# Kernel tuning notes

Hardware: AMD Instinct MI355X
Metric: run time of the kernel (lower is better)

The kernel has to match this reference:

```python
import jax, jax.numpy as jnp
import numpy as np

B = 32768
NUM_DENSE = 13
PAD_DENSE = 16  # 13 padded up to multiple of 8
T = 26          # number of categorical tables
V = 100000      # cardinality per table
E = 128         # embedding_dim
BOTTOM_DIMS = [512, 256, 128]
TOP_DIMS = [1024, 1024, 512, 256, 1]
N_FEAT = T + 1  # 27 feature vectors entering interaction
PAIR = N_FEAT * (N_FEAT - 1) // 2  # 351
TOP_IN = PAIR + E   # 479
TOP_PAD = 480       # padded to multiple of 8


def _glorot(key, fan_in, fan_out):
    s = np.sqrt(2.0 / (fan_in + fan_out))
    return jax.random.normal(key, (fan_in, fan_out), jnp.float32) * s


def setup_inputs() -> dict:
    key = jax.random.key(0)
    ks = jax.random.split(key, 32)
    inp = {
        "numerical": jax.random.normal(ks[0], (B, NUM_DENSE), jnp.float32),
        "cat_features": jax.random.randint(ks[1], (B, T), 0, V, jnp.int32),
        "emb_tables": jax.random.normal(ks[2], (T, V, E), jnp.float32) * 0.01,
    }
    # bottom MLP: 16 -> 512 -> 256 -> 128 (all relu)
    d_in = PAD_DENSE
    for i, d in enumerate(BOTTOM_DIMS):
        inp[f"bw{i}"] = _glorot(ks[3 + 2 * i], d_in, d)
        inp[f"bb{i}"] = jax.random.normal(ks[4 + 2 * i], (d,), jnp.float32) * np.sqrt(1.0 / d)
        d_in = d
    # top MLP: 480 -> 1024 -> 1024 -> 512 -> 256 -> 1 (relu except last)
    d_in = TOP_PAD
    for i, d in enumerate(TOP_DIMS):
        inp[f"tw{i}"] = _glorot(ks[12 + 2 * i], d_in, d)
        inp[f"tb{i}"] = jax.random.normal(ks[13 + 2 * i], (d,), jnp.float32) * np.sqrt(1.0 / d)
        d_in = d
    return inp


def reference(numerical, cat_features, emb_tables,
              bw0, bb0, bw1, bb1, bw2, bb2,
              tw0, tb0, tw1, tb1, tw2, tb2, tw3, tb3, tw4, tb4):
    b = numerical.shape[0]
    # --- bottom MLP (dense features padded with zeros to 16) ---
    x = jnp.pad(numerical, ((0, 0), (0, PAD_DENSE - NUM_DENSE)))
    for w, bias in ((bw0, bb0), (bw1, bb1), (bw2, bb2)):
        x = jax.nn.relu(x @ w + bias)
    bottom_out = x  # [B, E]
    # --- multi-table embedding gather: emb_tables[t][cat[:, t]] ---
    emb_out = jax.vmap(lambda tab, idx: tab[idx], in_axes=(0, 1), out_axes=1)(
        emb_tables, cat_features)  # [B, T, E]
    # --- dot interaction ---
    feats = jnp.concatenate([bottom_out[:, None, :], emb_out], axis=1)  # [B, 27, E]
    Z = jnp.einsum('bnd,bmd->bnm', feats, feats)  # [B, 27, 27]
    iu, ju = jnp.triu_indices(N_FEAT, k=1)
    pair = Z[:, iu, ju]  # [B, 351]
    x = jnp.concatenate(
        [bottom_out, pair, jnp.zeros((b, TOP_PAD - TOP_IN), feats.dtype)], axis=1)  # [B, 480]
    # --- top MLP (relu except last layer) ---
    tops = ((tw0, tb0), (tw1, tb1), (tw2, tb2), (tw3, tb3), (tw4, tb4))
    for i, (w, bias) in enumerate(tops):
        x = x @ w + bias
        if i < len(tops) - 1:
            x = jax.nn.relu(x)
    return x  # [B, 1] logits
```

## Files before the change

kernel.cpp:

```cpp
#include <hip/hip_runtime.h>

typedef __bf16 bf16;
typedef __bf16 bf16x4 __attribute__((ext_vector_type(4)));
typedef __bf16 bf16x8 __attribute__((ext_vector_type(8)));
typedef float f32x4 __attribute__((ext_vector_type(4)));

#define B_SZ 32768
#define T_CAT 26
#define V_SZ 100000
#define E_SZ 128

__device__ __forceinline__ void gload_lds16(const void* g, void* l) {
    __builtin_amdgcn_global_load_lds(
        (const __attribute__((address_space(1))) void*)g,
        (__attribute__((address_space(3))) void*)l, 16, 0, 0);
}

struct CJob { const float* W; bf16* Wt; int K, N, Kp, blk0, tk; };
struct CJobs { CJob j[7]; };

__global__ __launch_bounds__(256) void convw_all(CJobs js) {
    __shared__ bf16 tile[64][66];
    const int b = blockIdx.x;
    int ji = 0;
#pragma unroll
    for (int k = 1; k < 7; ++k)
        if (b >= js.j[k].blk0) ji = k;
    const CJob J = js.j[ji];
    const int local = b - J.blk0;
    const int tn = local / J.tk;
    const int tkk = local - tn * J.tk;

    const int t = threadIdx.x;
    const int lx = t & 63;
    const int gy = t >> 6;

#pragma unroll
    for (int kk = 0; kk < 16; ++kk) {
        const int k = tkk * 64 + kk * 4 + gy;
        const int n = tn * 64 + lx;
        const float v = (k < J.K) ? J.W[(long)k * J.N + n] : 0.0f;
        tile[lx][kk * 4 + gy] = (bf16)v;
    }
    __syncthreads();
#pragma unroll
    for (int nn = 0; nn < 16; ++nn) {
        const int nloc = nn * 4 + gy;
        const int n = tn * 64 + nloc;
        const int k = tkk * 64 + lx;
        J.Wt[(long)n * J.Kp + k] = tile[nloc][lx];
    }
}

__global__ __launch_bounds__(256) void make_xpad(const float* __restrict__ num,
                                                 bf16* __restrict__ xp) {
    const int idx = blockIdx.x * 256 + threadIdx.x;
    const int b = idx >> 6, c = idx & 63;
    xp[idx] = (bf16)((c < 13) ? num[(long)b * 13 + c] : 0.0f);
}

template <int RELU>
__global__ __launch_bounds__(256) void gemm_bt(const bf16* __restrict__ A,
                                               const bf16* __restrict__ Bt,
                                               const float* __restrict__ bias,
                                               bf16* __restrict__ C,
                                               int M, int N, int K) {
    __shared__ __align__(16) bf16 As[128 * 64];
    __shared__ __align__(16) bf16 Bs[128 * 64];
    const int t = threadIdx.x;
    const int lane = t & 63;
    const int w = t >> 6;
    const int wm = w >> 1, wn = w & 1;
    const long row0 = (long)blockIdx.y * 128;
    const long col0 = (long)blockIdx.x * 128;

    const int srow = t >> 3;
    const int scol = (t & 7) * 8;
    const bf16* Ag = A + (row0 + srow) * (long)K + scol;
    const bf16* Bg = Bt + (col0 + srow) * (long)K + scol;
    bf16* AsB = &As[w * 512];
    bf16* BsB = &Bs[w * 512];

    f32x4 acc[4][4] = {};

    for (int k0 = 0; k0 < K; k0 += 64) {
#pragma unroll
        for (int q = 0; q < 4; ++q) {
            gload_lds16(Ag + (long)q * 32 * K + k0, AsB + q * 2048);
            gload_lds16(Bg + (long)q * 32 * K + k0, BsB + q * 2048);
        }
        __syncthreads();
#pragma unroll
        for (int s = 0; s < 2; ++s) {
            bf16x8 af[4], bv[4];
#pragma unroll
            for (int i = 0; i < 4; ++i)
                af[i] = *(const bf16x8*)&As[(wm * 64 + i * 16 + (lane & 15)) * 64 +
                                            s * 32 + (lane >> 4) * 8];
#pragma unroll
            for (int j = 0; j < 4; ++j)
                bv[j] = *(const bf16x8*)&Bs[(wn * 64 + j * 16 + (lane & 15)) * 64 +
                                            s * 32 + (lane >> 4) * 8];
#pragma unroll
            for (int i = 0; i < 4; ++i)
#pragma unroll
                for (int j = 0; j < 4; ++j)
                    acc[i][j] = __builtin_amdgcn_mfma_f32_16x16x32_bf16(
                        af[i], bv[j], acc[i][j], 0, 0, 0);
        }
        __syncthreads();
    }

    const int r4 = (lane >> 4) * 4;
    const int cn = lane & 15;
#pragma unroll
    for (int j = 0; j < 4; ++j) {
        const long col = col0 + wn * 64 + j * 16 + cn;
        const float bj = bias[col];
#pragma unroll
        for (int i = 0; i < 4; ++i) {
#pragma unroll
            for (int r = 0; r < 4; ++r) {
                const long row = row0 + wm * 64 + i * 16 + r4 + r;
                float v = acc[i][j][r] + bj;
                if (RELU) v = v > 0.0f ? v : 0.0f;
                C[row * (long)N + col] = (bf16)v;
            }
        }
    }
}

template <int RELU>
__global__ __launch_bounds__(512, 2) void gemm256(const bf16* __restrict__ A,
                                                  const bf16* __restrict__ Bt,
                                                  const float* __restrict__ bias,
                                                  bf16* __restrict__ C,
                                                  int M, int N, int K, int nbx) {
    __shared__ __align__(16) bf16 lds[4 * 2 * 8192];
    const int t = threadIdx.x;
    const int lane = t & 63;
    const int w = t >> 6;
    const int wm = w >> 2, wn = w & 3;

    const int nwg = gridDim.x;
    const int qch = nwg >> 3;
    const int swz = ((int)blockIdx.x & 7) * qch + ((int)blockIdx.x >> 3);
    const int bx = swz % nbx, by = swz / nbx;
    const long row0 = (long)by * 256;
    const long col0 = (long)bx * 256;

    const int NT = K >> 5;

    const int lr = lane >> 2;
    const int dslot = lane & 3;
    const int lrow0 = (w * 2 + 0) * 16 + lr;
    const int lrow1 = (w * 2 + 1) * 16 + lr;
    const int sl0 = dslot ^ ((lrow0 >> 1) & 3);
    const int sl1 = dslot ^ ((lrow1 >> 1) & 3);
    const bf16* Ag0 = A + (row0 + lrow0) * (long)K + sl0 * 8;
    const bf16* Ag1 = A + (row0 + lrow1) * (long)K + sl1 * 8;
    const bf16* Bg0 = Bt + (col0 + lrow0) * (long)K + sl0 * 8;
    const bf16* Bg1 = Bt + (col0 + lrow1) * (long)K + sl1 * 8;
    const int ldsRow0 = (w * 2 + 0) * 512;
    const int ldsRow1 = (w * 2 + 1) * 512;

#define STAGE_A(buf, kt)                                                   \
    do {                                                                   \
        const int _k0 = (kt) << 5;                                         \
        gload_lds16(Ag0 + _k0, &lds[((buf) * 2 + 0) * 8192 + ldsRow0]);    \
        gload_lds16(Ag1 + _k0, &lds[((buf) * 2 + 0) * 8192 + ldsRow1]);    \
    } while (0)
#define STAGE_B(buf, kt)                                                   \
    do {                                                                   \
        const int _k0 = (kt) << 5;                                         \
        gload_lds16(Bg0 + _k0, &lds[((buf) * 2 + 1) * 8192 + ldsRow0]);    \
        gload_lds16(Bg1 + _k0, &lds[((buf) * 2 + 1) * 8192 + ldsRow1]);    \
    } while (0)

    const int cm = lane & 15;
    const int kc = lane >> 4;
    int aoff[8], boff[4];
#pragma unroll
    for (int i = 0; i < 8; ++i) {
        const int r = wm * 128 + i * 16 + cm;
        aoff[i] = r * 32 + (kc ^ ((r >> 1) & 3)) * 8;
    }
#pragma unroll
    for (int j = 0; j < 4; ++j) {
        const int n = wn * 64 + j * 16 + cm;
        boff[j] = n * 32 + (kc ^ ((n >> 1) & 3)) * 8;
    }

    f32x4 acc[8][4] = {};

    STAGE_A(0, 0); STAGE_B(0, 0);
    STAGE_A(1, 1); STAGE_B(1, 1);
    STAGE_A(2, 2); STAGE_B(2, 2);

    for (int tt = 0; tt < NT; ++tt) {
        const int rem = NT - 1 - tt;
        const int sb = (tt + 3) & 3;
        const int sk = tt + 3;

        if (rem >= 2)      asm volatile("s_waitcnt vmcnt(8)" ::: "memory");
        else if (rem == 1) asm volatile("s_waitcnt vmcnt(4)" ::: "memory");
        else               asm volatile("s_waitcnt vmcnt(0)" ::: "memory");
        __builtin_amdgcn_s_barrier();

        const bf16* Ab = &lds[((tt & 3) * 2 + 0) * 8192];
        const bf16* Bb = &lds[((tt & 3) * 2 + 1) * 8192];

        bf16x8 bfr[4], af[4];
#pragma unroll
        for (int j = 0; j < 4; ++j) bfr[j] = *(const bf16x8*)&Bb[boff[j]];
#pragma unroll
        for (int i = 0; i < 4; ++i) af[i] = *(const bf16x8*)&Ab[aoff[i]];
        if (rem >= 3) STAGE_A(sb, sk);
        __builtin_amdgcn_s_barrier();
        __builtin_amdgcn_s_setprio(1);
#pragma unroll
        for (int i = 0; i < 4; ++i)
#pragma unroll
            for (int j = 0; j < 4; ++j)
                acc[i][j] = __builtin_amdgcn_mfma_f32_16x16x32_bf16(
                    af[i], bfr[j], acc[i][j], 0, 0, 0);
        __builtin_amdgcn_s_setprio(0);

        bf16x8 af2[4];
#pragma unroll
        for (int i = 0; i < 4; ++i) af2[i] = *(const bf16x8*)&Ab[aoff[4 + i]];
        if (rem >= 3) STAGE_B(sb, sk);
        __builtin_amdgcn_s_barrier();
        __builtin_amdgcn_s_setprio(1);
#pragma unroll
        for (int i = 0; i < 4; ++i)
#pragma unroll
            for (int j = 0; j < 4; ++j)
                acc[4 + i][j] = __builtin_amdgcn_mfma_f32_16x16x32_bf16(
                    af2[i], bfr[j], acc[4 + i][j], 0, 0, 0);
        __builtin_amdgcn_s_setprio(0);
    }
#undef STAGE_A
#undef STAGE_B

    const int r4 = kc * 4;
#pragma unroll
    for (int j = 0; j < 4; ++j) {
        const long col = col0 + wn * 64 + j * 16 + cm;
        const float bj = bias[col];
#pragma unroll
        for (int i = 0; i < 8; ++i) {
#pragma unroll
            for (int r = 0; r < 4; ++r) {
                const long row = row0 + wm * 128 + i * 16 + r4 + r;
                float v = acc[i][j][r] + bj;
                if (RELU) v = v > 0.0f ? v : 0.0f;
                C[row * (long)N + col] = (bf16)v;
            }
        }
    }
}

__global__ __launch_bounds__(256) void interact_k(const float* __restrict__ emb,
                                                  const int* __restrict__ cat,
                                                  const bf16* __restrict__ bottom,
                                                  bf16* __restrict__ top_in) {
    __shared__ float gram[4][32 * 32];
    __shared__ __align__(16) bf16 rowbuf[4][512];
    const int t = threadIdx.x;
    const int lane = t & 63;
    const int w = t >> 6;
    const long s = (long)blockIdx.x * 4 + w;

    const int rl = lane & 15;
    const int kg = lane >> 4;

    bf16x8 f[2][4];
#pragma unroll
    for (int i = 0; i < 2; ++i) {
        const int r = i * 16 + rl;
        const float* rowp = nullptr;
        if (r >= 1 && r <= 26) {
            const int idx = cat[s * T_CAT + (r - 1)];
            rowp = emb + ((long)(r - 1) * V_SZ + idx) * E_SZ;
        }
#pragma unroll
        for (int ks = 0; ks < 4; ++ks) {
            const int c = ks * 32 + kg * 8;
            bf16x8 v = {};
            if (r == 0) {
                v = *(const bf16x8*)(bottom + s * 128 + c);
            } else if (r <= 26) {
                const float4 v0 = *(const float4*)(rowp + c);
                const float4 v1 = *(const float4*)(rowp + c + 4);
                v[0]=(bf16)v0.x; v[1]=(bf16)v0.y; v[2]=(bf16)v0.z; v[3]=(bf16)v0.w;
                v[4]=(bf16)v1.x; v[5]=(bf16)v1.y; v[6]=(bf16)v1.z; v[7]=(bf16)v1.w;
            }
            f[i][ks] = v;
        }
    }

    f32x4 a00 = {}, a01 = {}, a11 = {};
#pragma unroll
    for (int ks = 0; ks < 4; ++ks) {
        a00 = __builtin_amdgcn_mfma_f32_16x16x32_bf16(f[0][ks], f[0][ks], a00, 0, 0, 0);
        a01 = __builtin_amdgcn_mfma_f32_16x16x32_bf16(f[0][ks], f[1][ks], a01, 0, 0, 0);
        a11 = __builtin_amdgcn_mfma_f32_16x16x32_bf16(f[1][ks], f[1][ks], a11, 0, 0, 0);
    }

    const int r4 = kg * 4;
#pragma unroll
    for (int r = 0; r < 4; ++r) {
        gram[w][(r4 + r) * 32 + rl]           = a00[r];
        gram[w][(r4 + r) * 32 + 16 + rl]      = a01[r];
        gram[w][(16 + r4 + r) * 32 + 16 + rl] = a11[r];
    }
    asm volatile("s_waitcnt lgkmcnt(0)" ::: "memory");
    __builtin_amdgcn_sched_barrier(0);

    if (lane < 16)
        ((bf16x8*)&rowbuf[w][0])[lane] = ((const bf16x8*)(bottom + s * 128))[lane];
    for (int p = lane; p < 351; p += 64) {
        int i = 0, b = 0;
        while (b + (26 - i) <= p) { b += 26 - i; ++i; }
        const int j = p - b + i + 1;
        rowbuf[w][128 + p] = (bf16)gram[w][i * 32 + j];
    }
    if (lane >= 31) rowbuf[w][448 + lane] = (bf16)0.0f;
    asm volatile("s_waitcnt lgkmcnt(0)" ::: "memory");
    __builtin_amdgcn_sched_barrier(0);

    *(bf16x8*)(top_in + s * 512 + lane * 8) = *(const bf16x8*)&rowbuf[w][lane * 8];
}

__global__ __launch_bounds__(256) void gemv_final(const bf16* __restrict__ A,
                                                  const float* __restrict__ w4,
                                                  const float* __restrict__ b4,
                                                  float* __restrict__ out) {
    const int t = threadIdx.x;
    const int lane = t & 63;
    const int w = t >> 6;
    const long m = (long)blockIdx.x * 4 + w;
    const bf16x4 v = *(const bf16x4*)(A + m * 256 + lane * 4);
    const float4 wv = *(const float4*)(w4 + lane * 4);
    float sum = (float)v[0] * wv.x + (float)v[1] * wv.y + (float)v[2] * wv.z +
                (float)v[3] * wv.w;
#pragma unroll
    for (int off = 32; off > 0; off >>= 1) sum += __shfl_down(sum, off);
    if (lane == 0) out[m] = sum + b4[0];
}

extern "C" void kernel_launch(void* const* d_in, const int* in_sizes, int n_in,
                              void* d_out, int out_size, void* d_ws, size_t ws_size,
                              hipStream_t stream) {
    const float* numerical = (const float*)d_in[0];
    const int*   cat       = (const int*)d_in[1];
    const float* emb       = (const float*)d_in[2];
    const float* bw0 = (const float*)d_in[3];
    const float* bb0 = (const float*)d_in[4];
    const float* bw1 = (const float*)d_in[5];
    const float* bb1 = (const float*)d_in[6];
    const float* bw2 = (const float*)d_in[7];
    const float* bb2 = (const float*)d_in[8];
    const float* tw0 = (const float*)d_in[9];
    const float* tb0 = (const float*)d_in[10];
    const float* tw1 = (const float*)d_in[11];
    const float* tb1 = (const float*)d_in[12];
    const float* tw2 = (const float*)d_in[13];
    const float* tb2 = (const float*)d_in[14];
    const float* tw3 = (const float*)d_in[15];
    const float* tb3 = (const float*)d_in[16];
    const float* tw4 = (const float*)d_in[17];
    const float* tb4 = (const float*)d_in[18];
    float* out = (float*)d_out;

    char* ws = (char*)d_ws;
    size_t off = 0;
    auto alloc = [&](size_t bytes) {
        char* p = ws + off;
        off += (bytes + 255) & ~(size_t)255;
        return p;
    };
    bf16* wt0b = (bf16*)alloc((size_t)512 * 64 * 2);
    bf16* wt1b = (bf16*)alloc((size_t)256 * 512 * 2);
    bf16* wt2b = (bf16*)alloc((size_t)128 * 256 * 2);
    bf16* wt0t = (bf16*)alloc((size_t)1024 * 512 * 2);
    bf16* wt1t = (bf16*)alloc((size_t)1024 * 1024 * 2);
    bf16* wt2t = (bf16*)alloc((size_t)512 * 1024 * 2);
    bf16* wt3t = (bf16*)alloc((size_t)256 * 512 * 2);
    bf16* xpad = (bf16*)alloc((size_t)B_SZ * 64 * 2);
    bf16* h0   = (bf16*)alloc((size_t)B_SZ * 512 * 2);
    bf16* h1   = (bf16*)alloc((size_t)B_SZ * 256 * 2);
    bf16* bot  = (bf16*)alloc((size_t)B_SZ * 128 * 2);
    bf16* t0   = (bf16*)alloc((size_t)B_SZ * 1024 * 2);
    bf16* t1   = (bf16*)alloc((size_t)B_SZ * 1024 * 2);
    bf16* top_in = h0;
    bf16* t2 = t0;
    bf16* t3 = t1;

    CJobs js;
    js.j[0] = {bw0, wt0b, 16, 512, 64, 0, 1};
    js.j[1] = {bw1, wt1b, 512, 256, 512, 8, 8};
    js.j[2] = {bw2, wt2b, 256, 128, 256, 40, 4};
    js.j[3] = {tw0, wt0t, 480, 1024, 512, 48, 8};
    js.j[4] = {tw1, wt1t, 1024, 1024, 1024, 176, 16};
    js.j[5] = {tw2, wt2t, 1024, 512, 1024, 432, 16};
    js.j[6] = {tw3, wt3t, 512, 256, 512, 560, 8};
    convw_all<<<592, 256, 0, stream>>>(js);

    make_xpad<<<(B_SZ * 64) / 256, 256, 0, stream>>>(numerical, xpad);

    gemm_bt<1><<<dim3(4, 256), 256, 0, stream>>>(xpad, wt0b, bb0, h0, B_SZ, 512, 64);
    gemm256<1><<<dim3(128), 512, 0, stream>>>(h0, wt1b, bb1, h1, B_SZ, 256, 512, 1);
    gemm_bt<1><<<dim3(1, 256), 256, 0, stream>>>(h1, wt2b, bb2, bot, B_SZ, 128, 256);

    interact_k<<<B_SZ / 4, 256, 0, stream>>>(emb, cat, bot, top_in);

    gemm256<1><<<dim3(4 * 128), 512, 0, stream>>>(top_in, wt0t, tb0, t0, B_SZ, 1024, 512, 4);
    gemm256<1><<<dim3(4 * 128), 512, 0, stream>>>(t0, wt1t, tb1, t1, B_SZ, 1024, 1024, 4);
    gemm256<1><<<dim3(2 * 128), 512, 0, stream>>>(t1, wt2t, tb2, t2, B_SZ, 512, 1024, 2);
    gemm256<1><<<dim3(128), 512, 0, stream>>>(t2, wt3t, tb3, t3, B_SZ, 256, 512, 1);

    gemv_final<<<B_SZ / 4, 256, 0, stream>>>(t3, tw4, tb4, out);
}
```

Before: 392.9 us.

## Restructure gemm256 mainloop into K=64 double-buffered tiles with phased staging

```diff
diff --git a/kernel.cpp b/kernel.cpp
--- a/kernel.cpp
+++ b/kernel.cpp
@@ -136,7 +136,7 @@
                                                   const float* __restrict__ bias,
                                                   bf16* __restrict__ C,
                                                   int M, int N, int K, int nbx) {
-    __shared__ __align__(16) bf16 lds[4 * 2 * 8192];
+    __shared__ __align__(16) bf16 lds[65536];
     const int t = threadIdx.x;
     const int lane = t & 63;
     const int w = t >> 6;
@@ -149,99 +149,92 @@
     const long row0 = (long)by * 256;
     const long col0 = (long)bx * 256;
 
-    const int NT = K >> 5;
-
-    const int lr = lane >> 2;
-    const int dslot = lane & 3;
-    const int lrow0 = (w * 2 + 0) * 16 + lr;
-    const int lrow1 = (w * 2 + 1) * 16 + lr;
-    const int sl0 = dslot ^ ((lrow0 >> 1) & 3);
-    const int sl1 = dslot ^ ((lrow1 >> 1) & 3);
-    const bf16* Ag0 = A + (row0 + lrow0) * (long)K + sl0 * 8;
-    const bf16* Ag1 = A + (row0 + lrow1) * (long)K + sl1 * 8;
-    const bf16* Bg0 = Bt + (col0 + lrow0) * (long)K + sl0 * 8;
-    const bf16* Bg1 = Bt + (col0 + lrow1) * (long)K + sl1 * 8;
-    const int ldsRow0 = (w * 2 + 0) * 512;
-    const int ldsRow1 = (w * 2 + 1) * 512;
-
-#define STAGE_A(buf, kt)                                                   \
+    const int NT = K >> 6;
+
+    const int srow = t >> 2;
+    const int scol = (t & 3) * 8;
+    const bf16* Ag = A + (row0 + srow) * (long)K + scol;
+    const bf16* Bg = Bt + (col0 + srow) * (long)K + scol;
+
+#define STG(BUF, MAT, KH, KT)                                              \
     do {                                                                   \
-        const int _k0 = (kt) << 5;                                         \
-        gload_lds16(Ag0 + _k0, &lds[((buf) * 2 + 0) * 8192 + ldsRow0]);    \
-        gload_lds16(Ag1 + _k0, &lds[((buf) * 2 + 0) * 8192 + ldsRow1]);    \
-    } while (0)
-#define STAGE_B(buf, kt)                                                   \
-    do {                                                                   \
-        const int _k0 = (kt) << 5;                                         \
-        gload_lds16(Bg0 + _k0, &lds[((buf) * 2 + 1) * 8192 + ldsRow0]);    \
-        gload_lds16(Bg1 + _k0, &lds[((buf) * 2 + 1) * 8192 + ldsRow1]);    \
+        const bf16* _g = ((MAT) ? Bg : Ag) + (long)(KT)*64 + (KH)*32;      \
+        bf16* _l = &lds[(BUF)*32768 + (MAT)*16384 + (KH)*8192 + w * 512];  \
+        gload_lds16(_g, _l);                                               \
+        gload_lds16(_g + 128 * (long)K, _l + 4096);                        \
     } while (0)
 
     const int cm = lane & 15;
     const int kc = lane >> 4;
-    int aoff[8], boff[4];
-#pragma unroll
-    for (int i = 0; i < 8; ++i) {
-        const int r = wm * 128 + i * 16 + cm;
-        aoff[i] = r * 32 + (kc ^ ((r >> 1) & 3)) * 8;
-    }
-#pragma unroll
-    for (int j = 0; j < 4; ++j) {
-        const int n = wn * 64 + j * 16 + cm;
-        boff[j] = n * 32 + (kc ^ ((n >> 1) & 3)) * 8;
-    }
-
+    const int abase = (wm * 128 + cm) * 32 + kc * 8;
+    const int bbase = 16384 + (wn * 64 + cm) * 32 + kc * 8;
+
+    bf16x8 bfr[4];
     f32x4 acc[8][4] = {};
 
-    STAGE_A(0, 0); STAGE_B(0, 0);
-    STAGE_A(1, 1); STAGE_B(1, 1);
-    STAGE_A(2, 2); STAGE_B(2, 2);
-
-    for (int tt = 0; tt < NT; ++tt) {
-        const int rem = NT - 1 - tt;
-        const int sb = (tt + 3) & 3;
-        const int sk = tt + 3;
-
-        if (rem >= 2)      asm volatile("s_waitcnt vmcnt(8)" ::: "memory");
-        else if (rem == 1) asm volatile("s_waitcnt vmcnt(4)" ::: "memory");
-        else               asm volatile("s_waitcnt vmcnt(0)" ::: "memory");
-        __builtin_amdgcn_s_barrier();
-
-        const bf16* Ab = &lds[((tt & 3) * 2 + 0) * 8192];
-        const bf16* Bb = &lds[((tt & 3) * 2 + 1) * 8192];
-
-        bf16x8 bfr[4], af[4];
-#pragma unroll
-        for (int j = 0; j < 4; ++j) bfr[j] = *(const bf16x8*)&Bb[boff[j]];
-#pragma unroll
-        for (int i = 0; i < 4; ++i) af[i] = *(const bf16x8*)&Ab[aoff[i]];
-        if (rem >= 3) STAGE_A(sb, sk);
-        __builtin_amdgcn_s_barrier();
-        __builtin_amdgcn_s_setprio(1);
-#pragma unroll
-        for (int i = 0; i < 4; ++i)
-#pragma unroll
-            for (int j = 0; j < 4; ++j)
-                acc[i][j] = __builtin_amdgcn_mfma_f32_16x16x32_bf16(
-                    af[i], bfr[j], acc[i][j], 0, 0, 0);
-        __builtin_amdgcn_s_setprio(0);
-
-        bf16x8 af2[4];
-#pragma unroll
-        for (int i = 0; i < 4; ++i) af2[i] = *(const bf16x8*)&Ab[aoff[4 + i]];
-        if (rem >= 3) STAGE_B(sb, sk);
-        __builtin_amdgcn_s_barrier();
-        __builtin_amdgcn_s_setprio(1);
-#pragma unroll
-        for (int i = 0; i < 4; ++i)
-#pragma unroll
-            for (int j = 0; j < 4; ++j)
-                acc[4 + i][j] = __builtin_amdgcn_mfma_f32_16x16x32_bf16(
-                    af2[i], bfr[j], acc[4 + i][j], 0, 0, 0);
-        __builtin_amdgcn_s_setprio(0);
-    }
-#undef STAGE_A
-#undef STAGE_B
+#define PH(BUFB, S, IH, LOADB, STAGE, WAIT)                                   \
+    do {                                                                      \
+        if (LOADB) {                                                          \
+            _Pragma("unroll") for (int j = 0; j < 4; ++j)                     \
+                bfr[j] = *(const bf16x8*)&lds[(BUFB) + bbase + (S)*8192 + j*512]; \
+        }                                                                     \
+        bf16x8 af[4];                                                         \
+        _Pragma("unroll") for (int i = 0; i < 4; ++i)                         \
+            af[i] = *(const bf16x8*)&lds[(BUFB) + abase + (S)*8192 + ((IH)*4+i)*512]; \
+        STAGE;                                                                \
+        WAIT;                                                                 \
+        asm volatile("" ::: "memory");                                       \
+        __builtin_amdgcn_s_barrier();                                        \
+        asm volatile("s_waitcnt lgkmcnt(0)" ::: "memory");                    \
+        __builtin_amdgcn_s_setprio(1);                                       \
+        _Pragma("unroll") for (int i = 0; i < 4; ++i)                         \
+            _Pragma("unroll") for (int j = 0; j < 4; ++j)                     \
+                acc[(IH)*4 + i][j] = __builtin_amdgcn_mfma_f32_16x16x32_bf16( \
+                    af[i], bfr[j], acc[(IH)*4 + i][j], 0, 0, 0);              \
+        __builtin_amdgcn_s_setprio(0);                                       \
+        asm volatile("" ::: "memory");                                       \
+        __builtin_amdgcn_s_barrier();                                        \
+        asm volatile("" ::: "memory");                                       \
+    } while (0)
+
+#define TILE(BUFB, S1, S2, S3, S4, W4)          \
+    PH(BUFB, 0, 0, 1, S1, ((void)0));           \
+    PH(BUFB, 0, 1, 0, S2, ((void)0));           \
+    PH(BUFB, 1, 0, 1, S3, ((void)0));           \
+    PH(BUFB, 1, 1, 0, S4, W4)
+
+#define VM6 asm volatile("s_waitcnt vmcnt(6)" ::: "memory")
+#define VM0 asm volatile("s_waitcnt vmcnt(0)" ::: "memory")
+#define NOP ((void)0)
+
+    STG(0, 1, 0, 0); STG(0, 0, 0, 0); STG(0, 1, 1, 0); STG(0, 0, 1, 0);
+    STG(1, 1, 0, 1); STG(1, 0, 0, 1); STG(1, 1, 1, 1);
+    VM6;
+    __builtin_amdgcn_s_barrier();
+
+    for (int tt = 0; tt + 3 < NT; tt += 2) {
+        TILE(0,
+             STG(1, 0, 1, tt + 1),
+             STG(0, 1, 0, tt + 2),
+             STG(0, 0, 0, tt + 2),
+             STG(0, 1, 1, tt + 2),
+             VM6);
+        TILE(32768,
+             STG(0, 0, 1, tt + 2),
+             STG(1, 1, 0, tt + 3),
+             STG(1, 0, 0, tt + 3),
+             STG(1, 1, 1, tt + 3),
+             VM6);
+    }
+    TILE(0, STG(1, 0, 1, NT - 1), NOP, NOP, NOP, VM0);
+    TILE(32768, NOP, NOP, NOP, NOP, NOP);
+
+#undef STG
+#undef PH
+#undef TILE
+#undef VM6
+#undef VM0
+#undef NOP
 
     const int r4 = kc * 4;
 #pragma unroll
```

New measurement: 388.6 us. About the same (-1.1%).

## Replace pipelined 256x256 GEMM with occupancy-based 256x128 tile kernel

Applied to the files above, without the earlier changes.

```diff
diff --git a/kernel.cpp b/kernel.cpp
--- a/kernel.cpp
+++ b/kernel.cpp
@@ -131,117 +131,68 @@
 }
 
 template <int RELU>
-__global__ __launch_bounds__(512, 2) void gemm256(const bf16* __restrict__ A,
-                                                  const bf16* __restrict__ Bt,
-                                                  const float* __restrict__ bias,
-                                                  bf16* __restrict__ C,
-                                                  int M, int N, int K, int nbx) {
-    __shared__ __align__(16) bf16 lds[4 * 2 * 8192];
+__global__ __launch_bounds__(512, 4) void gemm_bt2(const bf16* __restrict__ A,
+                                                   const bf16* __restrict__ Bt,
+                                                   const float* __restrict__ bias,
+                                                   bf16* __restrict__ C,
+                                                   int M, int N, int K, int nbx) {
+    __shared__ __align__(16) bf16 As[256 * 64];
+    __shared__ __align__(16) bf16 Bs[128 * 64];
     const int t = threadIdx.x;
     const int lane = t & 63;
     const int w = t >> 6;
-    const int wm = w >> 2, wn = w & 3;
+    const int wm = w >> 1, wn = w & 1;
 
     const int nwg = gridDim.x;
     const int qch = nwg >> 3;
     const int swz = ((int)blockIdx.x & 7) * qch + ((int)blockIdx.x >> 3);
     const int bx = swz % nbx, by = swz / nbx;
     const long row0 = (long)by * 256;
-    const long col0 = (long)bx * 256;
-
-    const int NT = K >> 5;
-
-    const int lr = lane >> 2;
-    const int dslot = lane & 3;
-    const int lrow0 = (w * 2 + 0) * 16 + lr;
-    const int lrow1 = (w * 2 + 1) * 16 + lr;
-    const int sl0 = dslot ^ ((lrow0 >> 1) & 3);
-    const int sl1 = dslot ^ ((lrow1 >> 1) & 3);
-    const bf16* Ag0 = A + (row0 + lrow0) * (long)K + sl0 * 8;
-    const bf16* Ag1 = A + (row0 + lrow1) * (long)K + sl1 * 8;
-    const bf16* Bg0 = Bt + (col0 + lrow0) * (long)K + sl0 * 8;
-    const bf16* Bg1 = Bt + (col0 + lrow1) * (long)K + sl1 * 8;
-    const int ldsRow0 = (w * 2 + 0) * 512;
-    const int ldsRow1 = (w * 2 + 1) * 512;
-
-#define STAGE_A(buf, kt)                                                   \
-    do {                                                                   \
-        const int _k0 = (kt) << 5;                                         \
-        gload_lds16(Ag0 + _k0, &lds[((buf) * 2 + 0) * 8192 + ldsRow0]);    \
-        gload_lds16(Ag1 + _k0, &lds[((buf) * 2 + 0) * 8192 + ldsRow1]);    \
-    } while (0)
-#define STAGE_B(buf, kt)                                                   \
-    do {                                                                   \
-        const int _k0 = (kt) << 5;                                         \
-        gload_lds16(Bg0 + _k0, &lds[((buf) * 2 + 1) * 8192 + ldsRow0]);    \
-        gload_lds16(Bg1 + _k0, &lds[((buf) * 2 + 1) * 8192 + ldsRow1]);    \
-    } while (0)
+    const long col0 = (long)bx * 128;
+
+    const int srow = t >> 3;
+    const int dslot = t & 7;
+    const int gsl = dslot ^ (srow & 7);
+    const bf16* Ag = A + (row0 + srow) * (long)K + gsl * 8;
+    const bf16* Bg = Bt + (col0 + srow) * (long)K + gsl * 8;
+    bf16* AsB = &As[w * 512];
+    bf16* BsB = &Bs[w * 512];
 
     const int cm = lane & 15;
     const int kc = lane >> 4;
-    int aoff[8], boff[4];
-#pragma unroll
-    for (int i = 0; i < 8; ++i) {
-        const int r = wm * 128 + i * 16 + cm;
-        aoff[i] = r * 32 + (kc ^ ((r >> 1) & 3)) * 8;
-    }
-#pragma unroll
-    for (int j = 0; j < 4; ++j) {
-        const int n = wn * 64 + j * 16 + cm;
-        boff[j] = n * 32 + (kc ^ ((n >> 1) & 3)) * 8;
-    }
-
-    f32x4 acc[8][4] = {};
-
-    STAGE_A(0, 0); STAGE_B(0, 0);
-    STAGE_A(1, 1); STAGE_B(1, 1);
-    STAGE_A(2, 2); STAGE_B(2, 2);
-
-    for (int tt = 0; tt < NT; ++tt) {
-        const int rem = NT - 1 - tt;
-        const int sb = (tt + 3) & 3;
-        const int sk = tt + 3;
-
-        if (rem >= 2)      asm volatile("s_waitcnt vmcnt(8)" ::: "memory");
-        else if (rem == 1) asm volatile("s_waitcnt vmcnt(4)" ::: "memory");
-        else               asm volatile("s_waitcnt vmcnt(0)" ::: "memory");
-        __builtin_amdgcn_s_barrier();
-
-        const bf16* Ab = &lds[((tt & 3) * 2 + 0) * 8192];
-        const bf16* Bb = &lds[((tt & 3) * 2 + 1) * 8192];
-
-        bf16x8 bfr[4], af[4];
-#pragma unroll
-        for (int j = 0; j < 4; ++j) bfr[j] = *(const bf16x8*)&Bb[boff[j]];
-#pragma unroll
-        for (int i = 0; i < 4; ++i) af[i] = *(const bf16x8*)&Ab[aoff[i]];
-        if (rem >= 3) STAGE_A(sb, sk);
-        __builtin_amdgcn_s_barrier();
-        __builtin_amdgcn_s_setprio(1);
-#pragma unroll
-        for (int i = 0; i < 4; ++i)
-#pragma unroll
-            for (int j = 0; j < 4; ++j)
-                acc[i][j] = __builtin_amdgcn_mfma_f32_16x16x32_bf16(
-                    af[i], bfr[j], acc[i][j], 0, 0, 0);
-        __builtin_amdgcn_s_setprio(0);
-
-        bf16x8 af2[4];
-#pragma unroll
-        for (int i = 0; i < 4; ++i) af2[i] = *(const bf16x8*)&Ab[aoff[4 + i]];
-        if (rem >= 3) STAGE_B(sb, sk);
-        __builtin_amdgcn_s_barrier();
-        __builtin_amdgcn_s_setprio(1);
-#pragma unroll
-        for (int i = 0; i < 4; ++i)
-#pragma unroll
-            for (int j = 0; j < 4; ++j)
-                acc[4 + i][j] = __builtin_amdgcn_mfma_f32_16x16x32_bf16(
-                    af2[i], bfr[j], acc[4 + i][j], 0, 0, 0);
-        __builtin_amdgcn_s_setprio(0);
-    }
-#undef STAGE_A
-#undef STAGE_B
+
+    f32x4 acc[4][4] = {};
+
+    for (int k0 = 0; k0 < K; k0 += 64) {
+#pragma unroll
+        for (int q = 0; q < 4; ++q)
+            gload_lds16(Ag + (long)q * 64 * K + k0, AsB + q * 4096);
+#pragma unroll
+        for (int q = 0; q < 2; ++q)
+            gload_lds16(Bg + (long)q * 64 * K + k0, BsB + q * 4096);
+        __syncthreads();
+#pragma unroll
+        for (int s = 0; s < 2; ++s) {
+            bf16x8 af[4], bv[4];
+#pragma unroll
+            for (int i = 0; i < 4; ++i) {
+                const int r = wm * 64 + i * 16 + cm;
+                af[i] = *(const bf16x8*)&As[r * 64 + (((s * 4 + kc) ^ (r & 7)) * 8)];
+            }
+#pragma unroll
+            for (int j = 0; j < 4; ++j) {
+                const int r = wn * 64 + j * 16 + cm;
+                bv[j] = *(const bf16x8*)&Bs[r * 64 + (((s * 4 + kc) ^ (r & 7)) * 8)];
+            }
+#pragma unroll
+            for (int i = 0; i < 4; ++i)
+#pragma unroll
+                for (int j = 0; j < 4; ++j)
+                    acc[i][j] = __builtin_amdgcn_mfma_f32_16x16x32_bf16(
+                        af[i], bv[j], acc[i][j], 0, 0, 0);
+        }
+        __syncthreads();
+    }
 
     const int r4 = kc * 4;
 #pragma unroll
@@ -249,10 +200,10 @@
         const long col = col0 + wn * 64 + j * 16 + cm;
         const float bj = bias[col];
 #pragma unroll
-        for (int i = 0; i < 8; ++i) {
+        for (int i = 0; i < 4; ++i) {
 #pragma unroll
             for (int r = 0; r < 4; ++r) {
-                const long row = row0 + wm * 128 + i * 16 + r4 + r;
+                const long row = row0 + wm * 64 + i * 16 + r4 + r;
                 float v = acc[i][j][r] + bj;
                 if (RELU) v = v > 0.0f ? v : 0.0f;
                 C[row * (long)N + col] = (bf16)v;
@@ -411,15 +362,15 @@
     make_xpad<<<(B_SZ * 64) / 256, 256, 0, stream>>>(numerical, xpad);
 
     gemm_bt<1><<<dim3(4, 256), 256, 0, stream>>>(xpad, wt0b, bb0, h0, B_SZ, 512, 64);
-    gemm256<1><<<dim3(128), 512, 0, stream>>>(h0, wt1b, bb1, h1, B_SZ, 256, 512, 1);
+    gemm_bt2<1><<<dim3(256), 512, 0, stream>>>(h0, wt1b, bb1, h1, B_SZ, 256, 512, 2);
     gemm_bt<1><<<dim3(1, 256), 256, 0, stream>>>(h1, wt2b, bb2, bot, B_SZ, 128, 256);
 
     interact_k<<<B_SZ / 4, 256, 0, stream>>>(emb, cat, bot, top_in);
 
-    gemm256<1><<<dim3(4 * 128), 512, 0, stream>>>(top_in, wt0t, tb0, t0, B_SZ, 1024, 512, 4);
-    gemm256<1><<<dim3(4 * 128), 512, 0, stream>>>(t0, wt1t, tb1, t1, B_SZ, 1024, 1024, 4);
-    gemm256<1><<<dim3(2 * 128), 512, 0, stream>>>(t1, wt2t, tb2, t2, B_SZ, 512, 1024, 2);
-    gemm256<1><<<dim3(128), 512, 0, stream>>>(t2, wt3t, tb3, t3, B_SZ, 256, 512, 1);
+    gemm_bt2<1><<<dim3(1024), 512, 0, stream>>>(top_in, wt0t, tb0, t0, B_SZ, 1024, 512, 8);
+    gemm_bt2<1><<<dim3(1024), 512, 0, stream>>>(t0, wt1t, tb1, t1, B_SZ, 1024, 1024, 8);
+    gemm_bt2<1><<<dim3(512), 512, 0, stream>>>(t1, wt2t, tb2, t2, B_SZ, 512, 1024, 4);
+    gemm_bt2<1><<<dim3(256), 512, 0, stream>>>(t2, wt3t, tb3, t3, B_SZ, 256, 512, 2);
 
     gemv_final<<<B_SZ / 4, 256, 0, stream>>>(t3, tw4, tb4, out);
 }
```

Measured after the change: 339.6 us. -13.6%, faster.
